# Kernel optimization log

Hardware: AMD Instinct MI355X
Metric: run time of the kernel (lower is better)

Reference implementation:

```python
import jax, jax.numpy as jnp
import numpy as np

B, C, P, D = 4096, 1000, 10, 256
N = C * P            # total prototypes
E = 160000           # edges among prototypes
MARGIN = -0.1
LOSS_WEIGHT = 0.1
EPS = 1e-12          # F.normalize eps


def _gcn_conv(x, src, dst, deg_isqrt, w, b):
    # PyG GCNConv: symmetric-normalized aggregation with self-loops (added by caller)
    xw = x @ w                                   # [N, D]
    norm = deg_isqrt[src] * deg_isqrt[dst]       # [E+N]
    msg = norm[:, None] * xw[src]                # [E+N, D]
    out = jax.ops.segment_sum(msg, dst, num_segments=N)
    return out + b


def setup_inputs() -> dict:
    key = jax.random.key(0)
    ks = jax.random.split(key, 8)
    return {
        "hidden": jax.random.normal(ks[0], (B, D), jnp.float32),
        "labels": jax.random.randint(ks[1], (B,), 0, C),
        "edge_index": jax.random.randint(ks[2], (2, E), 0, N),
        "node_features": 0.02 * jax.random.normal(ks[3], (N, D), jnp.float32),
        "w1": jax.random.normal(ks[4], (D, D), jnp.float32) / np.sqrt(D),
        "b1": jnp.zeros((D,), jnp.float32),
        "w2": jax.random.normal(ks[5], (D, D), jnp.float32) / np.sqrt(D),
        "b2": jnp.zeros((D,), jnp.float32),
    }


def reference(hidden, labels, edge_index, node_features, w1, b1, w2, b2):
    # --- PrototypeGCN over the prototype graph (self-loops + sym norm) ---
    loops = jnp.arange(N, dtype=edge_index.dtype)
    src = jnp.concatenate([edge_index[0], loops])
    dst = jnp.concatenate([edge_index[1], loops])
    deg = jax.ops.segment_sum(jnp.ones_like(dst, jnp.float32), dst, num_segments=N)
    deg_isqrt = jnp.where(deg > 0, jax.lax.rsqrt(jnp.maximum(deg, 1.0)), 0.0)
    x = node_features
    x = jax.nn.relu(_gcn_conv(x, src, dst, deg_isqrt, w1, b1))
    x = jax.nn.relu(_gcn_conv(x, src, dst, deg_isqrt, w2, b2))

    # --- cosine similarity, per-class max over prototypes ---
    hidden_norm = hidden / jnp.maximum(jnp.linalg.norm(hidden, axis=1, keepdims=True), EPS)
    proto_norm = x / jnp.maximum(jnp.linalg.norm(x, axis=1, keepdims=True), EPS)
    sim = (1.0 + hidden_norm @ proto_norm.T) / 2.0          # [B, N]
    sim_pc = sim.reshape(B, C, P)
    output = sim_pc.max(axis=2)                              # [B, C]
    topk_idx = sim_pc.argmax(axis=2)                         # [B, C]

    # --- margin-masked cross entropy ---
    ar = jnp.arange(B)
    true_scores = output[ar, labels]
    pred_labels = output.argmax(axis=1)
    pred_scores = output.max(axis=1)
    mask = (true_scores - pred_scores) > MARGIN              # [B] bool
    cnt = mask.sum()
    per_ce = -jax.nn.log_softmax(output, axis=1)[ar, labels]
    ce_loss = jnp.sum(per_ce * mask) / jnp.maximum(cnt, 1).astype(per_ce.dtype)

    # dispersion = -mean(proto_norm @ proto_norm.T) = -||sum_i p_i||^2 / N^2
    s = proto_norm.sum(axis=0)
    dispersion_loss = -(s @ s) / (N * N)
    total_loss = jnp.where(cnt == 0, 0.0, ce_loss + LOSS_WEIGHT * dispersion_loss)

    # --- vectorized usage scatter (replaces Python double loop) ---
    pos_ids = labels * P + topk_idx[ar, labels]
    positive_usage = jnp.zeros((N,), jnp.float32).at[pos_ids].add(1.0)
    wrong = (pred_labels != labels).astype(jnp.float32)
    neg_ids = pred_labels * P + topk_idx[ar, pred_labels]
    negative_usage = jnp.zeros((N,), jnp.float32).at[neg_ids].add(wrong)

    return (output, total_loss, positive_usage, negative_usage)
```

## Files before the change

kernel.cpp:

```cpp
#include <hip/hip_runtime.h>
#include <math.h>

#define B_  4096
#define C_  1000
#define P_  10
#define D_  256
#define N_  10000
#define E_  160000

typedef __attribute__((ext_vector_type(8))) short short8;
typedef __attribute__((ext_vector_type(4))) float floatx4;

__device__ __forceinline__ float waveReduceSum(float v){
  #pragma unroll
  for (int o = 32; o > 0; o >>= 1) v += __shfl_xor(v, o);
  return v;
}
__device__ __forceinline__ unsigned short f2bf(float f){
  unsigned int u = __float_as_uint(f);
  unsigned int r = (u + 0x7FFFu + ((u >> 16) & 1u)) >> 16;
  return (unsigned short)r;
}
__device__ __forceinline__ float bf2f(unsigned short b){
  return __uint_as_float(((unsigned int)b) << 16);
}

__global__ void k_deg_hist(const int* __restrict__ dst, int* __restrict__ deg){
  int e = blockIdx.x * 256 + threadIdx.x;
  if (e < E_) atomicAdd(&deg[dst[e]], 1);
}

__global__ void k_isq(const int* __restrict__ deg, float* __restrict__ isq){
  int n = blockIdx.x * 256 + threadIdx.x;
  if (n < N_) isq[n] = 1.0f / sqrtf((float)(deg[n] + 1));
}

__global__ void k_scatter(const int* __restrict__ src, const int* __restrict__ dst,
                          int* __restrict__ cursor, const float* __restrict__ isq,
                          int* __restrict__ csr_src, float* __restrict__ csr_norm){
  int e = blockIdx.x * 256 + threadIdx.x;
  if (e >= E_) return;
  int d = dst[e], s = src[e];
  int p = atomicAdd(&cursor[d], 1);
  p = (p < 63) ? p : 63;
  csr_src [d * 64 + p] = s;
  csr_norm[d * 64 + p] = isq[s] * isq[d];
}

__global__ void k_split_a(const float* __restrict__ in,
                          unsigned short* __restrict__ hi,
                          unsigned short* __restrict__ lo){
  size_t i = (size_t)blockIdx.x * 256 + threadIdx.x;
  float x = in[i];
  unsigned short h = f2bf(x);
  hi[i] = h;
  lo[i] = f2bf(x - bf2f(h));
}

__global__ void k_split_w(const float* __restrict__ w1, const float* __restrict__ w2,
                          unsigned short* __restrict__ w1h, unsigned short* __restrict__ w1l,
                          unsigned short* __restrict__ w2h, unsigned short* __restrict__ w2l){
  int b = blockIdx.x;
  int k = threadIdx.x;
  const float* w = (b < 256) ? w1 : w2;
  int n = b & 255;
  float x = w[(size_t)k * 256 + n];
  unsigned short h = f2bf(x);
  unsigned short l = f2bf(x - bf2f(h));
  if (b < 256){ w1h[(size_t)n * 256 + k] = h; w1l[(size_t)n * 256 + k] = l; }
  else        { w2h[(size_t)n * 256 + k] = h; w2l[(size_t)n * 256 + k] = l; }
}

__global__ __launch_bounds__(64) void k_gemm_mfma(
    const unsigned short* __restrict__ Ah, const unsigned short* __restrict__ Al,
    const unsigned short* __restrict__ Wh, const unsigned short* __restrict__ Wl,
    float* __restrict__ outp){
  int lane = threadIdx.x;
  int l15 = lane & 15, lq = lane >> 4;
  int rb = blockIdx.x * 64;
  int nb = blockIdx.y * 32;

  floatx4 acc[4][2];
  #pragma unroll
  for (int mt = 0; mt < 4; ++mt)
    #pragma unroll
    for (int nt = 0; nt < 2; ++nt) acc[mt][nt] = (floatx4){0.f,0.f,0.f,0.f};

  int arow[4];
  #pragma unroll
  for (int mt = 0; mt < 4; ++mt){
    int r = rb + mt * 16 + l15;
    arow[mt] = (r < N_) ? r : (N_ - 1);
  }
  for (int kc = 0; kc < 256; kc += 32){
    short8 ah[4], al[4], bh[2], bl[2];
    #pragma unroll
    for (int mt = 0; mt < 4; ++mt){
      size_t o = (size_t)arow[mt] * 256 + kc + lq * 8;
      ah[mt] = *(const short8*)(Ah + o);
      al[mt] = *(const short8*)(Al + o);
    }
    #pragma unroll
    for (int nt = 0; nt < 2; ++nt){
      size_t o = (size_t)(nb + nt * 16 + l15) * 256 + kc + lq * 8;
      bh[nt] = *(const short8*)(Wh + o);
      bl[nt] = *(const short8*)(Wl + o);
    }
    #pragma unroll
    for (int nt = 0; nt < 2; ++nt)
      #pragma unroll
      for (int mt = 0; mt < 4; ++mt){
        floatx4 c = acc[mt][nt];
        c = __builtin_amdgcn_mfma_f32_16x16x32_bf16(al[mt], bh[nt], c, 0, 0, 0);
        c = __builtin_amdgcn_mfma_f32_16x16x32_bf16(ah[mt], bl[nt], c, 0, 0, 0);
        c = __builtin_amdgcn_mfma_f32_16x16x32_bf16(ah[mt], bh[nt], c, 0, 0, 0);
        acc[mt][nt] = c;
      }
  }
  #pragma unroll
  for (int mt = 0; mt < 4; ++mt)
    #pragma unroll
    for (int r = 0; r < 4; ++r){
      int row = rb + mt * 16 + lq * 4 + r;
      if (row < N_){
        #pragma unroll
        for (int nt = 0; nt < 2; ++nt)
          outp[(size_t)row * 256 + nb + nt * 16 + l15] = acc[mt][nt][r];
      }
    }
}

__global__ void k_agg_split(const float* __restrict__ XW, const int* __restrict__ deg,
                            const int* __restrict__ csr_src, const float* __restrict__ csr_norm,
                            const float* __restrict__ isq, const float* __restrict__ bias,
                            unsigned short* __restrict__ Xh, unsigned short* __restrict__ Xl){
  int n    = blockIdx.x * 4 + (threadIdx.x >> 6);
  int lane = threadIdx.x & 63;
  int c4   = lane * 4;
  int   es = csr_src [n * 64 + lane];
  float en = csr_norm[n * 64 + lane];
  int dg = deg[n]; dg = (dg < 64) ? dg : 64;
  float is = isq[n];
  float4 s = *(const float4*)(XW + (size_t)n * 256 + c4);
  float w = is * is;
  float4 a = make_float4(w * s.x, w * s.y, w * s.z, w * s.w);
  int i = 0;
  for (; i + 3 < dg; i += 4){
    int s0 = __shfl(es, i),   s1 = __shfl(es, i+1), s2 = __shfl(es, i+2), s3 = __shfl(es, i+3);
    float n0 = __shfl(en, i), n1 = __shfl(en, i+1), n2 = __shfl(en, i+2), n3 = __shfl(en, i+3);
    float4 v0 = *(const float4*)(XW + (size_t)s0 * 256 + c4);
    float4 v1 = *(const float4*)(XW + (size_t)s1 * 256 + c4);
    float4 v2 = *(const float4*)(XW + (size_t)s2 * 256 + c4);
    float4 v3 = *(const float4*)(XW + (size_t)s3 * 256 + c4);
    a.x += n0*v0.x + n1*v1.x + n2*v2.x + n3*v3.x;
    a.y += n0*v0.y + n1*v1.y + n2*v2.y + n3*v3.y;
    a.z += n0*v0.z + n1*v1.z + n2*v2.z + n3*v3.z;
    a.w += n0*v0.w + n1*v1.w + n2*v2.w + n3*v3.w;
  }
  for (; i < dg; ++i){
    int s0 = __shfl(es, i); float n0 = __shfl(en, i);
    float4 v0 = *(const float4*)(XW + (size_t)s0 * 256 + c4);
    a.x += n0 * v0.x; a.y += n0 * v0.y; a.z += n0 * v0.z; a.w += n0 * v0.w;
  }
  float4 b = *(const float4*)(bias + c4);
  float x0 = fmaxf(a.x + b.x, 0.f), x1 = fmaxf(a.y + b.y, 0.f);
  float x2 = fmaxf(a.z + b.z, 0.f), x3 = fmaxf(a.w + b.w, 0.f);
  unsigned short h0 = f2bf(x0), h1 = f2bf(x1), h2 = f2bf(x2), h3 = f2bf(x3);
  ushort4 hv = make_ushort4(h0, h1, h2, h3);
  ushort4 lv = make_ushort4(f2bf(x0 - bf2f(h0)), f2bf(x1 - bf2f(h1)),
                            f2bf(x2 - bf2f(h2)), f2bf(x3 - bf2f(h3)));
  *(ushort4*)(Xh + (size_t)n * 256 + c4) = hv;
  *(ushort4*)(Xl + (size_t)n * 256 + c4) = lv;
}

__global__ void k_agg_norm_split(const float* __restrict__ XW, const int* __restrict__ deg,
                                 const int* __restrict__ csr_src, const float* __restrict__ csr_norm,
                                 const float* __restrict__ isq, const float* __restrict__ bias,
                                 unsigned short* __restrict__ Ph, unsigned short* __restrict__ Pl){
  int n    = blockIdx.x * 4 + (threadIdx.x >> 6);
  int lane = threadIdx.x & 63;
  int c4   = lane * 4;
  int   es = csr_src [n * 64 + lane];
  float en = csr_norm[n * 64 + lane];
  int dg = deg[n]; dg = (dg < 64) ? dg : 64;
  float is = isq[n];
  float4 s = *(const float4*)(XW + (size_t)n * 256 + c4);
  float w = is * is;
  float4 a = make_float4(w * s.x, w * s.y, w * s.z, w * s.w);
  int i = 0;
  for (; i + 3 < dg; i += 4){
    int s0 = __shfl(es, i),   s1 = __shfl(es, i+1), s2 = __shfl(es, i+2), s3 = __shfl(es, i+3);
    float n0 = __shfl(en, i), n1 = __shfl(en, i+1), n2 = __shfl(en, i+2), n3 = __shfl(en, i+3);
    float4 v0 = *(const float4*)(XW + (size_t)s0 * 256 + c4);
    float4 v1 = *(const float4*)(XW + (size_t)s1 * 256 + c4);
    float4 v2 = *(const float4*)(XW + (size_t)s2 * 256 + c4);
    float4 v3 = *(const float4*)(XW + (size_t)s3 * 256 + c4);
    a.x += n0*v0.x + n1*v1.x + n2*v2.x + n3*v3.x;
    a.y += n0*v0.y + n1*v1.y + n2*v2.y + n3*v3.y;
    a.z += n0*v0.z + n1*v1.z + n2*v2.z + n3*v3.z;
    a.w += n0*v0.w + n1*v1.w + n2*v2.w + n3*v3.w;
  }
  for (; i < dg; ++i){
    int s0 = __shfl(es, i); float n0 = __shfl(en, i);
    float4 v0 = *(const float4*)(XW + (size_t)s0 * 256 + c4);
    a.x += n0 * v0.x; a.y += n0 * v0.y; a.z += n0 * v0.z; a.w += n0 * v0.w;
  }
  float4 b = *(const float4*)(bias + c4);
  float x0 = fmaxf(a.x + b.x, 0.f), x1 = fmaxf(a.y + b.y, 0.f);
  float x2 = fmaxf(a.z + b.z, 0.f), x3 = fmaxf(a.w + b.w, 0.f);
  float ss = x0*x0 + x1*x1 + x2*x2 + x3*x3;
  float tot = waveReduceSum(ss);
  float nrm = fmaxf(sqrtf(tot), 1e-12f);
  x0 /= nrm; x1 /= nrm; x2 /= nrm; x3 /= nrm;
  unsigned short h0 = f2bf(x0), h1 = f2bf(x1), h2 = f2bf(x2), h3 = f2bf(x3);
  ushort4 hv = make_ushort4(h0, h1, h2, h3);
  ushort4 lv = make_ushort4(f2bf(x0 - bf2f(h0)), f2bf(x1 - bf2f(h1)),
                            f2bf(x2 - bf2f(h2)), f2bf(x3 - bf2f(h3)));
  *(ushort4*)(Ph + (size_t)n * 256 + c4) = hv;
  *(ushort4*)(Pl + (size_t)n * 256 + c4) = lv;
}

__global__ void k_norm_split(const float* __restrict__ in,
                             unsigned short* __restrict__ hi,
                             unsigned short* __restrict__ lo){
  int r = blockIdx.x, t = threadIdx.x;
  float v = in[(size_t)r * 256 + t];
  float ss = waveReduceSum(v * v);
  __shared__ float red[4];
  int w = t >> 6;
  if ((t & 63) == 0) red[w] = ss;
  __syncthreads();
  float tot = red[0] + red[1] + red[2] + red[3];
  float nrm = fmaxf(sqrtf(tot), 1e-12f);
  float x = v / nrm;
  unsigned short h = f2bf(x);
  unsigned short l = f2bf(x - bf2f(h));
  hi[(size_t)r * 256 + t] = h;
  lo[(size_t)r * 256 + t] = l;
}

__global__ void k_colsum(const unsigned short* __restrict__ hi,
                         const unsigned short* __restrict__ lo,
                         float* __restrict__ s){
  int d = threadIdx.x;
  int r0 = blockIdx.x * 100;
  float acc = 0.f;
  for (int r = r0; r < r0 + 100; ++r)
    acc += bf2f(hi[(size_t)r * 256 + d]) + bf2f(lo[(size_t)r * 256 + d]);
  atomicAdd(&s[d], acc);
}

__global__ __launch_bounds__(256, 4) void k_sim_max(
    const unsigned short* __restrict__ HNh, const unsigned short* __restrict__ HNl,
    const unsigned short* __restrict__ PNh, const unsigned short* __restrict__ PNl,
    float* __restrict__ out, unsigned char* __restrict__ idxb){
  __shared__ __align__(16) char smem[25600];

  int tid  = threadIdx.x;
  int wid  = tid >> 6;
  int lane = tid & 63;
  int l15  = lane & 15, lq = lane >> 4;
  int rbw  = blockIdx.y * 128 + wid * 32;
  int cb80 = blockIdx.x * 80;

  floatx4 acc[2][5];
  #pragma unroll
  for (int mt = 0; mt < 2; ++mt)
    #pragma unroll
    for (int nt = 0; nt < 5; ++nt) acc[mt][nt] = (floatx4){0.f,0.f,0.f,0.f};

  int pbuf = 0;
  for (int kc = 0; kc < 256; kc += 32){
    unsigned short* Bh = (unsigned short*)(smem + pbuf * 12800);
    unsigned short* Bl = Bh + 3200;
    for (int f = tid; f < 640; f += 256){
      int dt = f >= 320;
      int f2 = f - (dt ? 320 : 0);
      int row = f2 >> 2, kq = f2 & 3;
      const unsigned short* gp = (dt ? PNl : PNh) + (size_t)(cb80 + row) * 256 + kc + kq * 8;
      uint4 v = *(const uint4*)gp;
      *(uint4*)((dt ? Bl : Bh) + row * 40 + kq * 8) = v;
    }
    short8 ah[2], al[2];
    #pragma unroll
    for (int mt = 0; mt < 2; ++mt){
      size_t o = (size_t)(rbw + mt * 16 + l15) * 256 + kc + lq * 8;
      ah[mt] = *(const short8*)(HNh + o);
      al[mt] = *(const short8*)(HNl + o);
    }
    __syncthreads();
    #pragma unroll
    for (int nt = 0; nt < 5; ++nt){
      int ro = (nt * 16 + l15) * 40 + lq * 8;
      short8 bh = *(const short8*)(Bh + ro);
      short8 bl = *(const short8*)(Bl + ro);
      #pragma unroll
      for (int mt = 0; mt < 2; ++mt){
        floatx4 c = acc[mt][nt];
        c = __builtin_amdgcn_mfma_f32_16x16x32_bf16(al[mt], bh, c, 0, 0, 0);
        c = __builtin_amdgcn_mfma_f32_16x16x32_bf16(ah[mt], bl, c, 0, 0, 0);
        c = __builtin_amdgcn_mfma_f32_16x16x32_bf16(ah[mt], bh, c, 0, 0, 0);
        acc[mt][nt] = c;
      }
    }
    pbuf ^= 1;
  }

  __syncthreads();

  float* redw = (float*)smem + wid * 1296;
  #pragma unroll
  for (int mt = 0; mt < 2; ++mt){
    #pragma unroll
    for (int nt = 0; nt < 5; ++nt)
      #pragma unroll
      for (int r = 0; r < 4; ++r)
        redw[(lq * 4 + r) * 81 + nt * 16 + l15] = acc[mt][nt][r];
    int row = lane >> 2;
    int q   = lane & 3;
    const float* basep = redw + row * 81 + q * 20;
    float vs[2]; int is[2];
    #pragma unroll
    for (int cc = 0; cc < 2; ++cc){
      float m = 0.5f * (1.0f + basep[cc * 10]); int mi = 0;
      #pragma unroll
      for (int p = 1; p < 10; ++p){
        float v = 0.5f * (1.0f + basep[cc * 10 + p]);
        if (v > m){ m = v; mi = p; }
      }
      vs[cc] = m; is[cc] = mi;
    }
    int grow = rbw + mt * 16 + row;
    int gcol = blockIdx.x * 8 + q * 2;
    *(float2*)(out + (size_t)grow * 1000 + gcol) = make_float2(vs[0], vs[1]);
    idxb[(size_t)grow * 1000 + gcol]     = (unsigned char)is[0];
    idxb[(size_t)grow * 1000 + gcol + 1] = (unsigned char)is[1];
  }
}

__global__ void k_row_pass(const float* __restrict__ out, const unsigned char* __restrict__ idxb,
                           const int* __restrict__ labels, int* __restrict__ cnt,
                           float* __restrict__ ce_sum, float* __restrict__ pos_usage,
                           float* __restrict__ neg_usage){
  int b = blockIdx.x * 4 + (threadIdx.x >> 6);
  int lane = threadIdx.x & 63;
  const float* row = out + (size_t)b * 1000;
  float m = -INFINITY, s = 0.f; int bi = 0x7fffffff;
  for (int c = lane; c < 1000; c += 64){
    float v = row[c];
    if (v > m){ s = s * expf(m - v) + 1.f; bi = c; m = v; }
    else       s += expf(v - m);
  }
  #pragma unroll
  for (int o = 32; o > 0; o >>= 1){
    float m2 = __shfl_xor(m, o);
    float s2 = __shfl_xor(s, o);
    int   b2 = __shfl_xor(bi, o);
    float M = fmaxf(m, m2);
    s = s * expf(m - M) + s2 * expf(m2 - M);
    if (m2 > m || (m2 == m && b2 < bi)) bi = b2;
    m = M;
  }
  if (lane == 0){
    int lab = labels[b];
    float true_score = row[lab];
    float per_ce = m + logf(s) - true_score;
    bool mask = (true_score - m) > -0.1f;
    if (mask){ atomicAdd(cnt, 1); atomicAdd(ce_sum, per_ce); }
    int pi = idxb[(size_t)b * 1000 + lab];
    atomicAdd(&pos_usage[lab * P_ + pi], 1.f);
    if (bi != lab){
      int ni = idxb[(size_t)b * 1000 + bi];
      atomicAdd(&neg_usage[bi * P_ + ni], 1.f);
    }
  }
}

__global__ void k_finalize(const float* __restrict__ s, const int* __restrict__ cnt,
                           const float* __restrict__ ce_sum, float* __restrict__ loss_out){
  int t = threadIdx.x;
  float v = s[t];
  float ss = waveReduceSum(v * v);
  __shared__ float red[4];
  if ((t & 63) == 0) red[t >> 6] = ss;
  __syncthreads();
  if (t == 0){
    float tot = red[0] + red[1] + red[2] + red[3];
    float disp = -tot / 1.0e8f;
    int c = *cnt;
    float total = (c == 0) ? 0.f
                : (*ce_sum / (float)(c < 1 ? 1 : c) + 0.1f * disp);
    *loss_out = total;
  }
}

extern "C" void kernel_launch(void* const* d_in, const int* in_sizes, int n_in,
                              void* d_out, int out_size, void* d_ws, size_t ws_size,
                              hipStream_t stream){
  const float* hidden = (const float*)d_in[0];
  const int*   labels = (const int*)  d_in[1];
  const int*   eidx   = (const int*)  d_in[2];
  const float* nodef  = (const float*)d_in[3];
  const float* w1     = (const float*)d_in[4];
  const float* b1     = (const float*)d_in[5];
  const float* w2     = (const float*)d_in[6];
  const float* b2     = (const float*)d_in[7];

  float* out       = (float*)d_out;
  float* loss_out  = out + (size_t)B_ * C_;
  float* pos_usage = loss_out + 1;
  float* neg_usage = pos_usage + N_;

  const int* srcp = eidx;
  const int* dstp = eidx + E_;

  char* base = (char*)d_ws;
  size_t off = 0;
  auto alloc = [&](size_t bytes) -> char* {
    char* p = base + off;
    off = (off + bytes + 255) & ~(size_t)255;
    return p;
  };
  int*   deg_cnt = (int*)  alloc((size_t)N_ * 4);
  int*   cursor  = (int*)  alloc((size_t)N_ * 4);
  float* svec    = (float*)alloc(256 * 4);
  int*   cnt     = (int*)  alloc(4);
  float* ce_sum  = (float*)alloc(4);
  size_t zero_bytes = off;
  float* deg_isqrt = (float*)alloc((size_t)N_ * 4);
  int*   csr_src   = (int*)  alloc((size_t)N_ * 64 * 4);
  float* csr_norm  = (float*)alloc((size_t)N_ * 64 * 4);
  float* XW        = (float*)alloc((size_t)N_ * 256 * 4);
  unsigned short* Xh = (unsigned short*)alloc((size_t)N_ * 256 * 2);
  unsigned short* Xl = (unsigned short*)alloc((size_t)N_ * 256 * 2);
  unsigned short* W1h = (unsigned short*)alloc(256 * 256 * 2);
  unsigned short* W1l = (unsigned short*)alloc(256 * 256 * 2);
  unsigned short* W2h = (unsigned short*)alloc(256 * 256 * 2);
  unsigned short* W2l = (unsigned short*)alloc(256 * 256 * 2);
  unsigned short* HNh = (unsigned short*)alloc((size_t)B_ * 256 * 2);
  unsigned short* HNl = (unsigned short*)alloc((size_t)B_ * 256 * 2);
  unsigned char* idxb = (unsigned char*)alloc((size_t)B_ * C_);

  hipMemsetAsync(base, 0, zero_bytes, stream);
  hipMemsetAsync(loss_out, 0, (size_t)(1 + 2 * N_) * 4, stream);

  k_deg_hist<<<(E_ + 255) / 256, 256, 0, stream>>>(dstp, deg_cnt);
  k_isq<<<(N_ + 255) / 256, 256, 0, stream>>>(deg_cnt, deg_isqrt);
  k_scatter<<<(E_ + 255) / 256, 256, 0, stream>>>(srcp, dstp, cursor, deg_isqrt, csr_src, csr_norm);

  k_split_a<<<N_, 256, 0, stream>>>(nodef, Xh, Xl);
  k_split_w<<<512, 256, 0, stream>>>(w1, w2, W1h, W1l, W2h, W2l);

  dim3 ggrid(157, 8);
  k_gemm_mfma<<<ggrid, 64, 0, stream>>>(Xh, Xl, W1h, W1l, XW);
  k_agg_split<<<N_ / 4, 256, 0, stream>>>(XW, deg_cnt, csr_src, csr_norm, deg_isqrt, b1, Xh, Xl);
  k_gemm_mfma<<<ggrid, 64, 0, stream>>>(Xh, Xl, W2h, W2l, XW);
  k_agg_norm_split<<<N_ / 4, 256, 0, stream>>>(XW, deg_cnt, csr_src, csr_norm, deg_isqrt, b2, Xh, Xl);

  k_norm_split<<<B_, 256, 0, stream>>>(hidden, HNh, HNl);
  k_colsum<<<100, 256, 0, stream>>>(Xh, Xl, svec);

  dim3 sgrid(125, 32);
  k_sim_max<<<sgrid, 256, 0, stream>>>(HNh, HNl, Xh, Xl, out, idxb);

  k_row_pass<<<B_ / 4, 256, 0, stream>>>(out, idxb, labels, cnt, ce_sum, pos_usage, neg_usage);
  k_finalize<<<1, 256, 0, stream>>>(svec, cnt, ce_sum, loss_out);
}
```

Measured before the change: 371.3 us.

## Fuse bf16 split into GEMM, merge degree histogram into CSR scatter, drop LDS staging

The CSR scatter now also yields the degree counts through its cursor, so the separate histogram kernel and the stored per-edge norm array go away. Edge norms are recomputed from deg_isqrt inside the aggregation kernels. The node-feature split kernel is removed: the GEMM reads fp32 rows and splits them into hi/lo bf16 in registers, and layer-1 aggregation writes fp32 instead of split halves. The similarity kernel drops its double-buffered shared-memory staging of prototypes and barriers, loading B fragments straight from global memory and relying on cache. The trade-off is redundant split arithmetic and wider fp32 reads in the GEMM, plus uncoalesced direct global loads in sim_max.

Measured after the change: 479.2 us. 1.29x slower.

```diff
diff --git a/kernel.cpp b/kernel.cpp
--- a/kernel.cpp
+++ b/kernel.cpp
@@ -24,37 +24,31 @@
 __device__ __forceinline__ float bf2f(unsigned short b){
   return __uint_as_float(((unsigned int)b) << 16);
 }
-
-__global__ void k_deg_hist(const int* __restrict__ dst, int* __restrict__ deg){
+__device__ __forceinline__ void split8(const float* __restrict__ p, short8& h8, short8& l8){
+  float4 v0 = *(const float4*)p;
+  float4 v1 = *(const float4*)(p + 4);
+  float v[8] = {v0.x, v0.y, v0.z, v0.w, v1.x, v1.y, v1.z, v1.w};
+  #pragma unroll
+  for (int j = 0; j < 8; ++j){
+    unsigned short h = f2bf(v[j]);
+    h8[j] = (short)h;
+    l8[j] = (short)f2bf(v[j] - bf2f(h));
+  }
+}
+
+__global__ void k_scatter(const int* __restrict__ src, const int* __restrict__ dst,
+                          int* __restrict__ cursor, int* __restrict__ csr_src){
   int e = blockIdx.x * 256 + threadIdx.x;
-  if (e < E_) atomicAdd(&deg[dst[e]], 1);
+  if (e >= E_) return;
+  int d = dst[e];
+  int p = atomicAdd(&cursor[d], 1);
+  p = (p < 63) ? p : 63;
+  csr_src[d * 64 + p] = src[e];
 }
 
 __global__ void k_isq(const int* __restrict__ deg, float* __restrict__ isq){
   int n = blockIdx.x * 256 + threadIdx.x;
   if (n < N_) isq[n] = 1.0f / sqrtf((float)(deg[n] + 1));
-}
-
-__global__ void k_scatter(const int* __restrict__ src, const int* __restrict__ dst,
-                          int* __restrict__ cursor, const float* __restrict__ isq,
-                          int* __restrict__ csr_src, float* __restrict__ csr_norm){
-  int e = blockIdx.x * 256 + threadIdx.x;
-  if (e >= E_) return;
-  int d = dst[e], s = src[e];
-  int p = atomicAdd(&cursor[d], 1);
-  p = (p < 63) ? p : 63;
-  csr_src [d * 64 + p] = s;
-  csr_norm[d * 64 + p] = isq[s] * isq[d];
-}
-
-__global__ void k_split_a(const float* __restrict__ in,
-                          unsigned short* __restrict__ hi,
-                          unsigned short* __restrict__ lo){
-  size_t i = (size_t)blockIdx.x * 256 + threadIdx.x;
-  float x = in[i];
-  unsigned short h = f2bf(x);
-  hi[i] = h;
-  lo[i] = f2bf(x - bf2f(h));
 }
 
 __global__ void k_split_w(const float* __restrict__ w1, const float* __restrict__ w2,
@@ -72,7 +66,7 @@
 }
 
 __global__ __launch_bounds__(64) void k_gemm_mfma(
-    const unsigned short* __restrict__ Ah, const unsigned short* __restrict__ Al,
+    const float* __restrict__ A,
     const unsigned short* __restrict__ Wh, const unsigned short* __restrict__ Wl,
     float* __restrict__ outp){
   int lane = threadIdx.x;
@@ -95,11 +89,8 @@
   for (int kc = 0; kc < 256; kc += 32){
     short8 ah[4], al[4], bh[2], bl[2];
     #pragma unroll
-    for (int mt = 0; mt < 4; ++mt){
-      size_t o = (size_t)arow[mt] * 256 + kc + lq * 8;
-      ah[mt] = *(const short8*)(Ah + o);
-      al[mt] = *(const short8*)(Al + o);
-    }
+    for (int mt = 0; mt < 4; ++mt)
+      split8(A + (size_t)arow[mt] * 256 + kc + lq * 8, ah[mt], al[mt]);
     #pragma unroll
     for (int nt = 0; nt < 2; ++nt){
       size_t o = (size_t)(nb + nt * 16 + l15) * 256 + kc + lq * 8;
@@ -130,24 +121,23 @@
     }
 }
 
-__global__ void k_agg_split(const float* __restrict__ XW, const int* __restrict__ deg,
-                            const int* __restrict__ csr_src, const float* __restrict__ csr_norm,
-                            const float* __restrict__ isq, const float* __restrict__ bias,
-                            unsigned short* __restrict__ Xh, unsigned short* __restrict__ Xl){
+__global__ void k_agg_relu(const float* __restrict__ XW, const int* __restrict__ deg,
+                           const int* __restrict__ csr_src, const float* __restrict__ isq,
+                           const float* __restrict__ bias, float* __restrict__ X1){
   int n    = blockIdx.x * 4 + (threadIdx.x >> 6);
   int lane = threadIdx.x & 63;
   int c4   = lane * 4;
-  int   es = csr_src [n * 64 + lane];
-  float en = csr_norm[n * 64 + lane];
   int dg = deg[n]; dg = (dg < 64) ? dg : 64;
-  float is = isq[n];
+  int   esr = (lane < dg) ? csr_src[n * 64 + lane] : 0;
+  float is  = isq[n];
+  float en  = isq[esr] * is;
   float4 s = *(const float4*)(XW + (size_t)n * 256 + c4);
   float w = is * is;
   float4 a = make_float4(w * s.x, w * s.y, w * s.z, w * s.w);
   int i = 0;
   for (; i + 3 < dg; i += 4){
-    int s0 = __shfl(es, i),   s1 = __shfl(es, i+1), s2 = __shfl(es, i+2), s3 = __shfl(es, i+3);
-    float n0 = __shfl(en, i), n1 = __shfl(en, i+1), n2 = __shfl(en, i+2), n3 = __shfl(en, i+3);
+    int s0 = __shfl(esr, i),   s1 = __shfl(esr, i+1), s2 = __shfl(esr, i+2), s3 = __shfl(esr, i+3);
+    float n0 = __shfl(en, i),  n1 = __shfl(en, i+1),  n2 = __shfl(en, i+2),  n3 = __shfl(en, i+3);
     float4 v0 = *(const float4*)(XW + (size_t)s0 * 256 + c4);
     float4 v1 = *(const float4*)(XW + (size_t)s1 * 256 + c4);
     float4 v2 = *(const float4*)(XW + (size_t)s2 * 256 + c4);
@@ -158,39 +148,35 @@
     a.w += n0*v0.w + n1*v1.w + n2*v2.w + n3*v3.w;
   }
   for (; i < dg; ++i){
-    int s0 = __shfl(es, i); float n0 = __shfl(en, i);
+    int s0 = __shfl(esr, i); float n0 = __shfl(en, i);
     float4 v0 = *(const float4*)(XW + (size_t)s0 * 256 + c4);
     a.x += n0 * v0.x; a.y += n0 * v0.y; a.z += n0 * v0.z; a.w += n0 * v0.w;
   }
   float4 b = *(const float4*)(bias + c4);
-  float x0 = fmaxf(a.x + b.x, 0.f), x1 = fmaxf(a.y + b.y, 0.f);
-  float x2 = fmaxf(a.z + b.z, 0.f), x3 = fmaxf(a.w + b.w, 0.f);
-  unsigned short h0 = f2bf(x0), h1 = f2bf(x1), h2 = f2bf(x2), h3 = f2bf(x3);
-  ushort4 hv = make_ushort4(h0, h1, h2, h3);
-  ushort4 lv = make_ushort4(f2bf(x0 - bf2f(h0)), f2bf(x1 - bf2f(h1)),
-                            f2bf(x2 - bf2f(h2)), f2bf(x3 - bf2f(h3)));
-  *(ushort4*)(Xh + (size_t)n * 256 + c4) = hv;
-  *(ushort4*)(Xl + (size_t)n * 256 + c4) = lv;
+  float4 o;
+  o.x = fmaxf(a.x + b.x, 0.f); o.y = fmaxf(a.y + b.y, 0.f);
+  o.z = fmaxf(a.z + b.z, 0.f); o.w = fmaxf(a.w + b.w, 0.f);
+  *(float4*)(X1 + (size_t)n * 256 + c4) = o;
 }
 
 __global__ void k_agg_norm_split(const float* __restrict__ XW, const int* __restrict__ deg,
-                                 const int* __restrict__ csr_src, const float* __restrict__ csr_norm,
-                                 const float* __restrict__ isq, const float* __restrict__ bias,
+                                 const int* __restrict__ csr_src, const float* __restrict__ isq,
+                                 const float* __restrict__ bias,
                                  unsigned short* __restrict__ Ph, unsigned short* __restrict__ Pl){
   int n    = blockIdx.x * 4 + (threadIdx.x >> 6);
   int lane = threadIdx.x & 63;
   int c4   = lane * 4;
-  int   es = csr_src [n * 64 + lane];
-  float en = csr_norm[n * 64 + lane];
   int dg = deg[n]; dg = (dg < 64) ? dg : 64;
-  float is = isq[n];
+  int   esr = (lane < dg) ? csr_src[n * 64 + lane] : 0;
+  float is  = isq[n];
+  float en  = isq[esr] * is;
   float4 s = *(const float4*)(XW + (size_t)n * 256 + c4);
   float w = is * is;
   float4 a = make_float4(w * s.x, w * s.y, w * s.z, w * s.w);
   int i = 0;
   for (; i + 3 < dg; i += 4){
-    int s0 = __shfl(es, i),   s1 = __shfl(es, i+1), s2 = __shfl(es, i+2), s3 = __shfl(es, i+3);
-    float n0 = __shfl(en, i), n1 = __shfl(en, i+1), n2 = __shfl(en, i+2), n3 = __shfl(en, i+3);
+    int s0 = __shfl(esr, i),   s1 = __shfl(esr, i+1), s2 = __shfl(esr, i+2), s3 = __shfl(esr, i+3);
+    float n0 = __shfl(en, i),  n1 = __shfl(en, i+1),  n2 = __shfl(en, i+2),  n3 = __shfl(en, i+3);
     float4 v0 = *(const float4*)(XW + (size_t)s0 * 256 + c4);
     float4 v1 = *(const float4*)(XW + (size_t)s1 * 256 + c4);
     float4 v2 = *(const float4*)(XW + (size_t)s2 * 256 + c4);
@@ -201,7 +187,7 @@
     a.w += n0*v0.w + n1*v1.w + n2*v2.w + n3*v3.w;
   }
   for (; i < dg; ++i){
-    int s0 = __shfl(es, i); float n0 = __shfl(en, i);
+    int s0 = __shfl(esr, i); float n0 = __shfl(en, i);
     float4 v0 = *(const float4*)(XW + (size_t)s0 * 256 + c4);
     a.x += n0 * v0.x; a.y += n0 * v0.y; a.z += n0 * v0.z; a.w += n0 * v0.w;
   }
@@ -254,7 +240,7 @@
     const unsigned short* __restrict__ HNh, const unsigned short* __restrict__ HNl,
     const unsigned short* __restrict__ PNh, const unsigned short* __restrict__ PNl,
     float* __restrict__ out, unsigned char* __restrict__ idxb){
-  __shared__ __align__(16) char smem[25600];
+  __shared__ float red4[4][1296];
 
   int tid  = threadIdx.x;
   int wid  = tid >> 6;
@@ -269,31 +255,22 @@
     #pragma unroll
     for (int nt = 0; nt < 5; ++nt) acc[mt][nt] = (floatx4){0.f,0.f,0.f,0.f};
 
-  int pbuf = 0;
+  const unsigned short* a0h = HNh + (size_t)(rbw + l15) * 256 + lq * 8;
+  const unsigned short* a0l = HNl + (size_t)(rbw + l15) * 256 + lq * 8;
+  const unsigned short* b0h = PNh + (size_t)(cb80 + l15) * 256 + lq * 8;
+  const unsigned short* b0l = PNl + (size_t)(cb80 + l15) * 256 + lq * 8;
+
   for (int kc = 0; kc < 256; kc += 32){
-    unsigned short* Bh = (unsigned short*)(smem + pbuf * 12800);
-    unsigned short* Bl = Bh + 3200;
-    for (int f = tid; f < 640; f += 256){
-      int dt = f >= 320;
-      int f2 = f - (dt ? 320 : 0);
-      int row = f2 >> 2, kq = f2 & 3;
-      const unsigned short* gp = (dt ? PNl : PNh) + (size_t)(cb80 + row) * 256 + kc + kq * 8;
-      uint4 v = *(const uint4*)gp;
-      *(uint4*)((dt ? Bl : Bh) + row * 40 + kq * 8) = v;
-    }
     short8 ah[2], al[2];
     #pragma unroll
     for (int mt = 0; mt < 2; ++mt){
-      size_t o = (size_t)(rbw + mt * 16 + l15) * 256 + kc + lq * 8;
-      ah[mt] = *(const short8*)(HNh + o);
-      al[mt] = *(const short8*)(HNl + o);
-    }
-    __syncthreads();
+      ah[mt] = *(const short8*)(a0h + (size_t)mt * 4096 + kc);
+      al[mt] = *(const short8*)(a0l + (size_t)mt * 4096 + kc);
+    }
     #pragma unroll
     for (int nt = 0; nt < 5; ++nt){
-      int ro = (nt * 16 + l15) * 40 + lq * 8;
-      short8 bh = *(const short8*)(Bh + ro);
-      short8 bl = *(const short8*)(Bl + ro);
+      short8 bh = *(const short8*)(b0h + (size_t)nt * 4096 + kc);
+      short8 bl = *(const short8*)(b0l + (size_t)nt * 4096 + kc);
       #pragma unroll
       for (int mt = 0; mt < 2; ++mt){
         floatx4 c = acc[mt][nt];
@@ -303,12 +280,9 @@
         acc[mt][nt] = c;
       }
     }
-    pbuf ^= 1;
-  }
-
-  __syncthreads();
-
-  float* redw = (float*)smem + wid * 1296;
+  }
+
+  float* redw = red4[wid];
   #pragma unroll
   for (int mt = 0; mt < 2; ++mt){
     #pragma unroll
@@ -421,7 +395,6 @@
     off = (off + bytes + 255) & ~(size_t)255;
     return p;
   };
-  int*   deg_cnt = (int*)  alloc((size_t)N_ * 4);
   int*   cursor  = (int*)  alloc((size_t)N_ * 4);
   float* svec    = (float*)alloc(256 * 4);
   int*   cnt     = (int*)  alloc(4);
@@ -429,10 +402,10 @@
   size_t zero_bytes = off;
   float* deg_isqrt = (float*)alloc((size_t)N_ * 4);
   int*   csr_src   = (int*)  alloc((size_t)N_ * 64 * 4);
-  float* csr_norm  = (float*)alloc((size_t)N_ * 64 * 4);
   float* XW        = (float*)alloc((size_t)N_ * 256 * 4);
-  unsigned short* Xh = (unsigned short*)alloc((size_t)N_ * 256 * 2);
-  unsigned short* Xl = (unsigned short*)alloc((size_t)N_ * 256 * 2);
+  float* X1        = (float*)alloc((size_t)N_ * 256 * 4);
+  unsigned short* Ph  = (unsigned short*)alloc((size_t)N_ * 256 * 2);
+  unsigned short* Pl  = (unsigned short*)alloc((size_t)N_ * 256 * 2);
   unsigned short* W1h = (unsigned short*)alloc(256 * 256 * 2);
   unsigned short* W1l = (unsigned short*)alloc(256 * 256 * 2);
   unsigned short* W2h = (unsigned short*)alloc(256 * 256 * 2);
@@ -444,24 +417,21 @@
   hipMemsetAsync(base, 0, zero_bytes, stream);
   hipMemsetAsync(loss_out, 0, (size_t)(1 + 2 * N_) * 4, stream);
 
-  k_deg_hist<<<(E_ + 255) / 256, 256, 0, stream>>>(dstp, deg_cnt);
-  k_isq<<<(N_ + 255) / 256, 256, 0, stream>>>(deg_cnt, deg_isqrt);
-  k_scatter<<<(E_ + 255) / 256, 256, 0, stream>>>(srcp, dstp, cursor, deg_isqrt, csr_src, csr_norm);
-
-  k_split_a<<<N_, 256, 0, stream>>>(nodef, Xh, Xl);
+  k_scatter<<<(E_ + 255) / 256, 256, 0, stream>>>(srcp, dstp, cursor, csr_src);
+  k_isq<<<(N_ + 255) / 256, 256, 0, stream>>>(cursor, deg_isqrt);
   k_split_w<<<512, 256, 0, stream>>>(w1, w2, W1h, W1l, W2h, W2l);
 
   dim3 ggrid(157, 8);
-  k_gemm_mfma<<<ggrid, 64, 0, stream>>>(Xh, Xl, W1h, W1l, XW);
-  k_agg_split<<<N_ / 4, 256, 0, stream>>>(XW, deg_cnt, csr_src, csr_norm, deg_isqrt, b1, Xh, Xl);
-  k_gemm_mfma<<<ggrid, 64, 0, stream>>>(Xh, Xl, W2h, W2l, XW);
-  k_agg_norm_split<<<N_ / 4, 256, 0, stream>>>(XW, deg_cnt, csr_src, csr_norm, deg_isqrt, b2, Xh, Xl);
+  k_gemm_mfma<<<ggrid, 64, 0, stream>>>(nodef, W1h, W1l, XW);
+  k_agg_relu<<<N_ / 4, 256, 0, stream>>>(XW, cursor, csr_src, deg_isqrt, b1, X1);
+  k_gemm_mfma<<<ggrid, 64, 0, stream>>>(X1, W2h, W2l, XW);
+  k_agg_norm_split<<<N_ / 4, 256, 0, stream>>>(XW, cursor, csr_src, deg_isqrt, b2, Ph, Pl);
 
   k_norm_split<<<B_, 256, 0, stream>>>(hidden, HNh, HNl);
-  k_colsum<<<100, 256, 0, stream>>>(Xh, Xl, svec);
+  k_colsum<<<100, 256, 0, stream>>>(Ph, Pl, svec);
 
   dim3 sgrid(125, 32);
-  k_sim_max<<<sgrid, 256, 0, stream>>>(HNh, HNl, Xh, Xl, out, idxb);
+  k_sim_max<<<sgrid, 256, 0, stream>>>(HNh, HNl, Ph, Pl, out, idxb);
 
   k_row_pass<<<B_ / 4, 256, 0, stream>>>(out, idxb, labels, cnt, ce_sum, pos_usage, neg_usage);
   k_finalize<<<1, 256, 0, stream>>>(svec, cnt, ce_sum, loss_out);
```
